# Kernel optimization log

Measured on AMD Instinct MI355X. Metric: run time of the kernel, lower is better.

Reference implementation:

```python
import jax, jax.numpy as jnp
import numpy as np

NB, NLOC, NALL, NNEI, A_SEL = 1, 512, 640, 96, 20
N_DIM, E_DIM, A_DIM, AXIS = 128, 64, 64, 4
EDGE_INFO = 2 * N_DIM + E_DIM          # 320
SYM = AXIS * (E_DIM + N_DIM)           # 768, cal_1_dim
ANGLE = A_DIM + N_DIM + 2 * E_DIM      # 320, angle_dim


def setup_inputs() -> dict:
    key = jax.random.key(0)
    ks = jax.random.split(key, 16)
    nrm = lambda k, sh, s=1.0: jax.random.normal(k, sh, dtype=jnp.float32) * s

    def lin(k, din, dout, s=0.05):
        k1, k2 = jax.random.split(k)
        return nrm(k1, (din, dout), s), nrm(k2, (dout,), s)

    inp = {}
    inp["g1_ext"] = nrm(ks[0], (NB, NALL, N_DIM))
    inp["g2"] = nrm(ks[1], (NB, NLOC, NNEI, E_DIM))
    inp["h2"] = nrm(ks[2], (NB, NLOC, NNEI, 3))
    inp["angle_embed"] = nrm(ks[3], (NB, NLOC, A_SEL, A_SEL, A_DIM))
    inp["sw"] = jax.random.uniform(ks[4], (NB, NLOC, NNEI), dtype=jnp.float32)
    inp["a_sw"] = jax.random.uniform(ks[5], (NB, NLOC, A_SEL), dtype=jnp.float32)
    inp["w_self"], inp["b_self"] = lin(ks[6], N_DIM, N_DIM)
    inp["w_proj"] = nrm(ks[7], (E_DIM, N_DIM), 0.05)  # proj_g1g2, bias=False
    inp["w_lin1"], inp["b_lin1"] = lin(ks[8], SYM, N_DIM)
    inp["w_edge1"], inp["b_edge1"] = lin(ks[9], EDGE_INFO, N_DIM)
    inp["w_lin2"], inp["b_lin2"] = lin(ks[10], EDGE_INFO, E_DIM)
    inp["w_ang"], inp["b_ang"] = lin(ks[11], ANGLE, A_DIM)
    inp["w_ga1"], inp["b_ga1"] = lin(ks[12], ANGLE, E_DIM)
    inp["w_ga2"], inp["b_ga2"] = lin(ks[13], E_DIM, E_DIM)
    inp["nlist"] = jax.random.randint(ks[14], (NB, NLOC, NNEI), 0, NALL)
    inp["nlist_mask"] = jnp.ones((NB, NLOC, NNEI), dtype=bool)
    inp["a_nlist_mask"] = jnp.ones((NB, NLOC, A_SEL), dtype=bool)
    return inp


def _sym_op(g, h2, mask, sw, axis):
    # symmetrization_op: _cal_hg (smooth, use_sqrt_nnei) followed by _cal_grrg
    # g: nb x nloc x nnei x d, h2: nb x nloc x nnei x 3
    g = jnp.where(mask[..., None], g, 0.0) * sw[..., None]
    inv = np.float32(1.0 / np.sqrt(g.shape[2]))
    hg = jnp.einsum('blnt,blnd->bltd', h2, g) * inv
    grrg = jnp.einsum('bltd,blta->blda', hg, hg[..., :axis])  # nb x nloc x d x axis
    return grrg.reshape(grrg.shape[0], grrg.shape[1], -1)


def reference(g1_ext, g2, h2, angle_embed, sw, a_sw,
              w_self, b_self, w_proj, w_lin1, b_lin1, w_edge1, b_edge1,
              w_lin2, b_lin2, w_ang, b_ang, w_ga1, b_ga1, w_ga2, b_ga2,
              nlist, nlist_mask, a_nlist_mask):
    act = jax.nn.silu
    nb, nloc, nnei, e_dim = g2.shape
    n_dim = g1_ext.shape[-1]
    a_sel = angle_embed.shape[2]
    g1 = g1_ext[:, :nloc]
    # _make_nei_g1: gather neighbor node features, nb x nloc x nnei x n_dim
    gg1 = jnp.take_along_axis(
        g1_ext, nlist.reshape(nb, nloc * nnei, 1), axis=1
    ).reshape(nb, nloc, nnei, n_dim)
    maskf = nlist_mask[..., None]
    swf = sw[..., None]

    g1_update = [g1]
    # node self mlp
    g1_update.append(act(g1 @ w_self + b_self))
    # conv update: masked+switched gg1 times projected g2, mean over nnei
    gg1_ms = jnp.where(maskf, gg1, 0.0) * swf
    g1_update.append(jnp.sum((g2 @ w_proj) * gg1_ms, axis=2) / np.float32(nnei))
    # symmetrized axis-neuron update
    sym = jnp.concatenate(
        [_sym_op(g2, h2, nlist_mask, sw, AXIS),
         _sym_op(gg1, h2, nlist_mask, sw, AXIS)], axis=-1)
    g1_update.append(act(sym @ w_lin1 + b_lin1))
    # edge info: [tiled g1, gg1, g2] -> 2*n_dim + e_dim
    edge_info = jnp.concatenate(
        [jnp.broadcast_to(g1[:, :, None, :], (nb, nloc, nnei, n_dim)), gg1, g2],
        axis=-1)
    g1_edge = act(edge_info @ w_edge1 + b_edge1) * swf
    g1_update.append(jnp.sum(g1_edge, axis=2) / np.float32(nnei))
    # res_avg
    g1_new = sum(g1_update) / np.float32(np.sqrt(len(g1_update)))

    g2_update = [g2, act(edge_info @ w_lin2 + b_lin2)]

    # angle branch: angle_dim = a_dim + n_dim + 2*e_dim
    g2a = jnp.where(a_nlist_mask[..., None], g2[:, :, :a_sel, :], 0.0)
    ang = jnp.concatenate([
        angle_embed,
        jnp.broadcast_to(g1[:, :, None, None, :], (nb, nloc, a_sel, a_sel, n_dim)),
        jnp.broadcast_to(g2a[:, :, :, None, :], (nb, nloc, a_sel, a_sel, e_dim)),
        jnp.broadcast_to(g2a[:, :, None, :, :], (nb, nloc, a_sel, a_sel, e_dim)),
    ], axis=-1)
    a_new = (angle_embed + act(ang @ w_ang + b_ang)) / np.float32(np.sqrt(2.0))

    # angle -> edge message, switch-weighted on both angle axes, mean over one axis
    ang_w = ang * a_sw[:, :, :, None, None] * a_sw[:, :, None, :, None]
    g2_ang = jnp.sum(act(ang_w @ w_ga1 + b_ga1), axis=3) / np.float32(a_sel)
    g2_ang_full = jnp.concatenate(
        [g2_ang, jnp.zeros((nb, nloc, nnei - a_sel, e_dim), g2.dtype)], axis=2)
    g2_update.append(act(g2_ang_full @ w_ga2 + b_ga2))
    g2_new = sum(g2_update) / np.float32(np.sqrt(len(g2_update)))

    return g1_new, g2_new, h2, a_new
```

## Files before the change

kernel.cpp:

```cpp
#include <hip/hip_runtime.h>
#include <hip/hip_bf16.h>

#define NLOC 512
#define NALL 640
#define NNEI 96
#define ASEL 20
#define NDIM 128
#define EDIM 64
#define ADIM 64

typedef short bf16x8 __attribute__((ext_vector_type(8)));
typedef float f32x4 __attribute__((ext_vector_type(4)));
typedef unsigned short ushort8 __attribute__((ext_vector_type(8)));
typedef unsigned short ushort4_t __attribute__((ext_vector_type(4)));

__device__ __forceinline__ unsigned short f2bf(float f) {
    unsigned int u = __float_as_uint(f);
    unsigned int r = (u + 0x7FFFu + ((u >> 16) & 1u)) >> 16;
    return (unsigned short)r;
}
__device__ __forceinline__ float bf2f(unsigned short u) {
    return __uint_as_float(((unsigned int)u) << 16);
}
__device__ __forceinline__ float silu(float x) { return x / (1.0f + __expf(-x)); }

__device__ __forceinline__ void cvt8_store(unsigned short* dst, const float* src) {
    float4 f0 = *(const float4*)src;
    float4 f1 = *(const float4*)(src + 4);
    ushort8 v;
    v[0] = f2bf(f0.x); v[1] = f2bf(f0.y); v[2] = f2bf(f0.z); v[3] = f2bf(f0.w);
    v[4] = f2bf(f1.x); v[5] = f2bf(f1.y); v[6] = f2bf(f1.z); v[7] = f2bf(f1.w);
    *(ushort8*)dst = v;
}

__global__ void prep_bt2(const float* __restrict__ w_ang, const float* __restrict__ w_ga1,
                         const float* __restrict__ w_edge1, const float* __restrict__ w_lin2,
                         const float* __restrict__ w_proj, const float* __restrict__ w_self,
                         unsigned short* __restrict__ bt_ae, unsigned short* __restrict__ bt_g2e,
                         unsigned short* __restrict__ bt_sm, unsigned short* __restrict__ bt_pij) {
    int idx = blockIdx.x * 256 + threadIdx.x;
    if (idx < 8192) {
        int k = idx & 63, n = idx >> 6;
        bt_ae[idx] = f2bf((n < 64) ? w_ang[k * 64 + n] : w_ga1[k * 64 + (n - 64)]);
    } else if (idx < 32768) {
        int id2 = idx - 8192;
        int k = id2 & 63, n = id2 >> 6;
        float v;
        if (n < 128)      v = w_edge1[(256 + k) * 128 + n];
        else if (n < 192) v = w_lin2[(256 + k) * 64 + (n - 128)];
        else if (n < 256) v = 0.0f;
        else              v = w_proj[k * 128 + (n - 256)];
        bt_g2e[id2] = f2bf(v);
    } else if (idx < 114688) {
        int id3 = idx - 32768;
        int k = id3 & 127, n = id3 >> 7;
        float v;
        if (n < 128)      v = w_edge1[k * 128 + n];
        else if (n < 192) v = w_lin2[k * 64 + (n - 128)];
        else if (n < 320) v = w_edge1[(128 + k) * 128 + (n - 192)];
        else if (n < 384) v = w_lin2[(128 + k) * 64 + (n - 320)];
        else if (n < 512) { int c = n - 384;
            v = (c < 64) ? w_ang[(64 + k) * 64 + c] : w_ga1[(64 + k) * 64 + (c - 64)]; }
        else              v = w_self[k * 128 + (n - 512)];
        bt_sm[id3] = f2bf(v);
    } else {
        int id4 = idx - 114688;
        int k = id4 & 63, n = id4 >> 6;
        float v;
        if (n < 128) v = (n < 64) ? w_ang[(192 + k) * 64 + n] : w_ga1[(192 + k) * 64 + (n - 64)];
        else { int c = n - 128;
            v = (c < 64) ? w_ang[(256 + k) * 64 + c] : w_ga1[(256 + k) * 64 + (c - 64)]; }
        bt_pij[id4] = f2bf(v);
    }
}

__global__ __launch_bounds__(256) void gemm_small(
    const float* __restrict__ g1_ext, const unsigned short* __restrict__ bt_sm,
    const float* __restrict__ b_self, float* __restrict__ P1a, float* __restrict__ g1self,
    float* __restrict__ E1, float* __restrict__ E2) {
    const int m0 = blockIdx.x * 128;
    const int ntile = blockIdx.y;
    __shared__ __align__(16) unsigned short Asl[128 * 136];
    __shared__ __align__(16) unsigned short Bsl[128 * 136];
    const int tid = threadIdx.x;
#pragma unroll
    for (int u = 0; u < 8; u++) {
        int g = tid + u * 256;
        int row = g >> 4, seg = g & 15;
        cvt8_store(&Asl[row * 136 + seg * 8], g1_ext + (m0 + row) * 128 + seg * 8);
        *(ushort8*)&Bsl[row * 136 + seg * 8] =
            *(const ushort8*)&bt_sm[(ntile * 128 + row) * 128 + seg * 8];
    }
    __syncthreads();
    const int lane = tid & 63, wid = tid >> 6;
    const int wr = wid >> 1, wc = wid & 1;
    const int r15 = lane & 15, kg = lane >> 4;
    f32x4 acc[4][4] = {};
#pragma unroll
    for (int h = 0; h < 4; h++) {
        bf16x8 afr[4], bfr[4];
#pragma unroll
        for (int mi = 0; mi < 4; mi++)
            afr[mi] = *(const bf16x8*)&Asl[(wr * 64 + mi * 16 + r15) * 136 + h * 32 + kg * 8];
#pragma unroll
        for (int ni = 0; ni < 4; ni++)
            bfr[ni] = *(const bf16x8*)&Bsl[(wc * 64 + ni * 16 + r15) * 136 + h * 32 + kg * 8];
#pragma unroll
        for (int mi = 0; mi < 4; mi++)
#pragma unroll
            for (int ni = 0; ni < 4; ni++)
                acc[mi][ni] = __builtin_amdgcn_mfma_f32_16x16x32_bf16(afr[mi], bfr[ni], acc[mi][ni], 0, 0, 0);
    }
#pragma unroll
    for (int mi = 0; mi < 4; mi++) {
        int rbase = m0 + wr * 64 + mi * 16 + kg * 4;
#pragma unroll
        for (int ni = 0; ni < 4; ni++) {
            int gc = ntile * 128 + wc * 64 + ni * 16 + r15;
#pragma unroll
            for (int t2 = 0; t2 < 4; t2++) {
                int a = rbase + t2;
                float z = acc[mi][ni][t2];
                if (gc < 192) { if (a < 512) E1[a * 192 + gc] = z; }
                else if (gc < 384) E2[a * 192 + (gc - 192)] = z;
                else if (gc < 512) { if (a < 512) P1a[a * 128 + (gc - 384)] = z; }
                else { if (a < 512) g1self[a * 128 + (gc - 512)] = silu(z + b_self[gc - 512]); }
            }
        }
    }
}

__global__ __launch_bounds__(256) void gemm_pij(
    const float* __restrict__ g2, const unsigned short* __restrict__ bt_pij,
    unsigned short* __restrict__ P_i, unsigned short* __restrict__ P_j,
    unsigned short* __restrict__ P_jT) {
    const int m0 = blockIdx.x * 128;
    const int ntile = blockIdx.y;
    __shared__ __align__(16) unsigned short Asl[128 * 72];
    const int tid = threadIdx.x;
#pragma unroll
    for (int u = 0; u < 4; u++) {
        int g = tid + u * 256;
        int row = g >> 3, seg = g & 7;
        int li = m0 + row, l = li / 20, i = li - l * 20;
        cvt8_store(&Asl[row * 72 + seg * 8], g2 + (l * 96 + i) * 64 + seg * 8);
    }
    __syncthreads();
    const int lane = tid & 63, wid = tid >> 6;
    const int wr = wid >> 1, wc = wid & 1;
    const int r15 = lane & 15, kg = lane >> 4;
    f32x4 acc[4][4] = {};
#pragma unroll
    for (int h = 0; h < 2; h++) {
        bf16x8 afr[4], bfr[4];
#pragma unroll
        for (int mi = 0; mi < 4; mi++)
            afr[mi] = *(const bf16x8*)&Asl[(wr * 64 + mi * 16 + r15) * 72 + h * 32 + kg * 8];
#pragma unroll
        for (int ni = 0; ni < 4; ni++)
            bfr[ni] = *(const bf16x8*)&bt_pij[(ntile * 128 + wc * 64 + ni * 16 + r15) * 64 + h * 32 + kg * 8];
#pragma unroll
        for (int mi = 0; mi < 4; mi++)
#pragma unroll
            for (int ni = 0; ni < 4; ni++)
                acc[mi][ni] = __builtin_amdgcn_mfma_f32_16x16x32_bf16(afr[mi], bfr[ni], acc[mi][ni], 0, 0, 0);
    }
    unsigned short* Pout = (ntile == 0) ? P_i : P_j;
#pragma unroll
    for (int mi = 0; mi < 4; mi++) {
        int rbase = m0 + wr * 64 + mi * 16 + kg * 4;
#pragma unroll
        for (int ni = 0; ni < 4; ni++) {
            int c = wc * 64 + ni * 16 + r15;
#pragma unroll
            for (int t2 = 0; t2 < 4; t2++) {
                unsigned short v = f2bf(acc[mi][ni][t2]);
                int li = rbase + t2;
                Pout[li * 128 + c] = v;
                if (ntile == 1) {
                    int l = li / 20, j = li - l * 20;
                    P_jT[(l * 128 + c) * 20 + j] = v;
                }
            }
        }
    }
}

__global__ void k_sym(const float* __restrict__ g1_ext, const float* __restrict__ g2,
                      const float* __restrict__ h2, const float* __restrict__ sw,
                      const int* __restrict__ nlist, const float* __restrict__ w_lin1,
                      const float* __restrict__ b_lin1, float* __restrict__ term4) {
    int l = blockIdx.x, t = threadIdx.x;
    __shared__ float h2s[96 * 3];
    __shared__ float sws[96];
    __shared__ int nls[96];
    __shared__ float hg[3 * 192];
    __shared__ float symv[768];
    __shared__ float red[128];
    if (t < 96) { sws[t] = sw[l * 96 + t]; nls[t] = nlist[l * 96 + t]; }
    for (int p = t; p < 288; p += 256) h2s[p] = h2[l * 288 + p];
    __syncthreads();
    const float inv = 0.1020620726f;
    for (int p = t; p < 576; p += 256) {
        float acc = 0.0f;
        if (p < 192) {
            int tt = p >> 6, d = p & 63;
            for (int n = 0; n < 96; n++)
                acc += h2s[n * 3 + tt] * g2[(l * 96 + n) * 64 + d] * sws[n];
            hg[tt * 192 + d] = acc * inv;
        } else {
            int q = p - 192;
            int tt = q >> 7, d = q & 127;
            for (int n = 0; n < 96; n++)
                acc += h2s[n * 3 + tt] * g1_ext[nls[n] * 128 + d] * sws[n];
            hg[tt * 192 + 64 + d] = acc * inv;
        }
    }
    __syncthreads();
    for (int p = t; p < 768; p += 256) {
        float acc = 0.0f;
        if (p < 256) {
            int d = p >> 2, a = p & 3;
            for (int tt = 0; tt < 3; tt++) acc += hg[tt * 192 + d] * hg[tt * 192 + a];
        } else {
            int q = p - 256;
            int d = q >> 2, a = q & 3;
            for (int tt = 0; tt < 3; tt++) acc += hg[tt * 192 + 64 + d] * hg[tt * 192 + 64 + a];
        }
        symv[p] = acc;
    }
    __syncthreads();
    {
        int col = t & 127, half = t >> 7;
        float acc = 0.0f;
        int k0 = half * 384;
#pragma unroll 8
        for (int k = k0; k < k0 + 384; k++) acc += symv[k] * w_lin1[k * 128 + col];
        if (half) red[col] = acc;
        __syncthreads();
        if (!half) term4[l * 128 + col] = silu(acc + red[col] + b_lin1[col]);
    }
}

__global__ __launch_bounds__(256) void angle_main(
    const float* __restrict__ ae, const unsigned short* __restrict__ bt_ae,
    const float* __restrict__ P1a, const unsigned short* __restrict__ P_i,
    const unsigned short* __restrict__ P_j, const unsigned short* __restrict__ P_jT,
    const float* __restrict__ a_sw,
    const float* __restrict__ b_ang, const float* __restrict__ b_ga1,
    float* __restrict__ g2acc, float* __restrict__ a_new_out) {
    const int m0 = blockIdx.x * 128;
    __shared__ __align__(16) unsigned short Asl[128 * 72];
    const int tid = threadIdx.x;
#pragma unroll
    for (int u = 0; u < 4; u++) {
        int g = tid + u * 256;
        int row = g >> 3, seg = g & 7;
        cvt8_store(&Asl[row * 72 + seg * 8], ae + (m0 + row) * 64 + seg * 8);
    }
    __syncthreads();
    const int lane = tid & 63, wid = tid >> 6;
    const int r15 = lane & 15, kg = lane >> 4;
    f32x4 accA[2][4] = {};
    f32x4 accB[2][4] = {};
#pragma unroll
    for (int h = 0; h < 2; h++) {
        bf16x8 afr[2], bfrA[4], bfrB[4];
#pragma unroll
        for (int mi = 0; mi < 2; mi++)
            afr[mi] = *(const bf16x8*)&Asl[(wid * 32 + mi * 16 + r15) * 72 + h * 32 + kg * 8];
#pragma unroll
        for (int ni = 0; ni < 4; ni++) {
            bfrA[ni] = *(const bf16x8*)&bt_ae[(ni * 16 + r15) * 64 + h * 32 + kg * 8];
            bfrB[ni] = *(const bf16x8*)&bt_ae[(64 + ni * 16 + r15) * 64 + h * 32 + kg * 8];
        }
#pragma unroll
        for (int mi = 0; mi < 2; mi++)
#pragma unroll
            for (int ni = 0; ni < 4; ni++) {
                accA[mi][ni] = __builtin_amdgcn_mfma_f32_16x16x32_bf16(bfrA[ni], afr[mi], accA[mi][ni], 0, 0, 0);
                accB[mi][ni] = __builtin_amdgcn_mfma_f32_16x16x32_bf16(afr[mi], bfrB[ni], accB[mi][ni], 0, 0, 0);
            }
    }
#pragma unroll
    for (int mi = 0; mi < 2; mi++) {
        int r = m0 + wid * 32 + mi * 16 + r15;
        int l = r / 400;
        int rem = r - l * 400;
        int i = rem / 20;
        int j = rem - i * 20;
        const float* p1b = P1a + l * 128;
        const unsigned short* pib = P_i + (l * 20 + i) * 128;
        const unsigned short* pjb = P_j + (l * 20 + j) * 128;
        int lr = r - m0;
#pragma unroll
        for (int ni = 0; ni < 4; ni++) {
            int n0 = ni * 16 + kg * 4;
            f32x4 p1v = *(const f32x4*)&p1b[n0];
            ushort4_t piv = *(const ushort4_t*)&pib[n0];
            ushort4_t pjv = *(const ushort4_t*)&pjb[n0];
            ushort4_t aev = *(const ushort4_t*)&Asl[lr * 72 + n0];
            f32x4 bbv = *(const f32x4*)&b_ang[n0];
            f32x4 outv;
#pragma unroll
            for (int t2 = 0; t2 < 4; t2++) {
                float z = accA[mi][ni][t2] + p1v[t2] + bf2f(piv[t2]) + bf2f(pjv[t2]);
                outv[t2] = (bf2f(aev[t2]) + silu(z + bbv[t2])) * 0.70710678f;
            }
            *(f32x4*)&a_new_out[r * 64 + n0] = outv;
        }
    }
#pragma unroll
    for (int mi = 0; mi < 2; mi++) {
        int rbase = m0 + wid * 32 + mi * 16 + kg * 4;
        int l = rbase / 400;
        int rem = rbase - l * 400;
        int i = rem / 20;
        int j0 = rem - i * 20;
        const float* p1b = P1a + l * 128;
        const unsigned short* pib = P_i + (l * 20 + i) * 128;
        float swi = a_sw[l * 20 + i];
        f32x4 swjv = *(const f32x4*)&a_sw[l * 20 + j0];
#pragma unroll
        for (int ni = 0; ni < 4; ni++) {
            int c = 64 + ni * 16 + r15;
            int cc = c - 64;
            float base = p1b[c] + bf2f(pib[c]);
            float bb = b_ga1[cc];
            ushort4_t pjtv = *(const ushort4_t*)&P_jT[(l * 128 + c) * 20 + j0];
            float part = 0.0f;
#pragma unroll
            for (int t2 = 0; t2 < 4; t2++) {
                float z = accB[mi][ni][t2] + base + bf2f(pjtv[t2]);
                part += silu(swi * swjv[t2] * z + bb);
            }
            atomicAdd(&g2acc[(l * 20 + i) * 64 + cc], part);
        }
    }
}

__global__ void k_f2(const float* __restrict__ g2ang_acc, const float* __restrict__ w_ga2,
                     const float* __restrict__ b_ga2, float* __restrict__ yga2) {
    int l = blockIdx.x, t = threadIdx.x;
    __shared__ float gs[20 * 64];
    for (int p = t; p < 1280; p += 256) gs[p] = g2ang_acc[l * 1280 + p] * 0.05f;
    __syncthreads();
    for (int p = t; p < 1280; p += 256) {
        int i = p >> 6, c = p & 63;
        float acc = b_ga2[c];
#pragma unroll 8
        for (int k = 0; k < 64; k++) acc += gs[i * 64 + k] * w_ga2[k * 64 + c];
        yga2[l * 1280 + p] = silu(acc);
    }
}

__global__ __launch_bounds__(256) void edge_main(
    const float* __restrict__ g1_ext, const float* __restrict__ g2, const float* __restrict__ sw,
    const int* __restrict__ nlist, const unsigned short* __restrict__ bt_g2e,
    const float* __restrict__ E1, const float* __restrict__ E2,
    const float* __restrict__ b_edge1, const float* __restrict__ b_lin2,
    const float* __restrict__ b_ga2, const float* __restrict__ yga2,
    float* __restrict__ g1_acc3, float* __restrict__ g1_acc5, float* __restrict__ g2_new_out) {
    const int m0 = blockIdx.x * 128;
    const int ntile = blockIdx.y;
    __shared__ __align__(16) unsigned short Asl[128 * 72];
    const int tid = threadIdx.x;
#pragma unroll
    for (int u = 0; u < 4; u++) {
        int g = tid + u * 256;
        int row = g >> 3, seg = g & 7;
        cvt8_store(&Asl[row * 72 + seg * 8], g2 + (m0 + row) * 64 + seg * 8);
    }
    __syncthreads();
    const int lane = tid & 63, wid = tid >> 6;
    const int r15 = lane & 15, kg = lane >> 4;
    if (ntile == 1) {
        f32x4 acc[2][4] = {};
#pragma unroll
        for (int h = 0; h < 2; h++) {
            bf16x8 afr[2], bfr[4];
#pragma unroll
            for (int mi = 0; mi < 2; mi++)
                afr[mi] = *(const bf16x8*)&Asl[(wid * 32 + mi * 16 + r15) * 72 + h * 32 + kg * 8];
#pragma unroll
            for (int ni = 0; ni < 4; ni++)
                bfr[ni] = *(const bf16x8*)&bt_g2e[(128 + ni * 16 + r15) * 64 + h * 32 + kg * 8];
#pragma unroll
            for (int mi = 0; mi < 2; mi++)
#pragma unroll
                for (int ni = 0; ni < 4; ni++)
                    acc[mi][ni] = __builtin_amdgcn_mfma_f32_16x16x32_bf16(bfr[ni], afr[mi], acc[mi][ni], 0, 0, 0);
        }
#pragma unroll
        for (int mi = 0; mi < 2; mi++) {
            int r = m0 + wid * 32 + mi * 16 + r15;
            int l = r / 96;
            int nn = r - l * 96;
            const float* e1 = E1 + l * 192 + 128;
            const float* e2 = E2 + nlist[r] * 192 + 128;
            bool hasyg = (nn < ASEL);
            const float* yg = yga2 + (l * 20 + nn) * 64;
            int lr = r - m0;
#pragma unroll
            for (int ni = 0; ni < 4; ni++) {
                int n0 = ni * 16 + kg * 4;
                f32x4 e1v = *(const f32x4*)&e1[n0];
                f32x4 e2v = *(const f32x4*)&e2[n0];
                f32x4 bbv = *(const f32x4*)&b_lin2[n0];
                f32x4 bg2 = *(const f32x4*)&b_ga2[n0];
                ushort4_t g2v = *(const ushort4_t*)&Asl[lr * 72 + n0];
                f32x4 outv;
#pragma unroll
                for (int t2 = 0; t2 < 4; t2++) {
                    float z = acc[mi][ni][t2] + e1v[t2] + e2v[t2];
                    float y = silu(z + bbv[t2]);
                    float ygv = hasyg ? yg[n0 + t2] : silu(bg2[t2]);
                    outv[t2] = (bf2f(g2v[t2]) + y + ygv) * 0.57735027f;
                }
                *(f32x4*)&g2_new_out[r * 64 + n0] = outv;
            }
        }
    } else {
        const int wr = wid >> 1, wc = wid & 1;
        f32x4 acc[4][4] = {};
#pragma unroll
        for (int h = 0; h < 2; h++) {
            bf16x8 afr[4], bfr[4];
#pragma unroll
            for (int mi = 0; mi < 4; mi++)
                afr[mi] = *(const bf16x8*)&Asl[(wr * 64 + mi * 16 + r15) * 72 + h * 32 + kg * 8];
#pragma unroll
            for (int ni = 0; ni < 4; ni++)
                bfr[ni] = *(const bf16x8*)&bt_g2e[(ntile * 128 + wc * 64 + ni * 16 + r15) * 64 + h * 32 + kg * 8];
#pragma unroll
            for (int mi = 0; mi < 4; mi++)
#pragma unroll
                for (int ni = 0; ni < 4; ni++)
                    acc[mi][ni] = __builtin_amdgcn_mfma_f32_16x16x32_bf16(afr[mi], bfr[ni], acc[mi][ni], 0, 0, 0);
        }
#pragma unroll
        for (int mi = 0; mi < 4; mi++) {
            int rbase = m0 + wr * 64 + mi * 16 + kg * 4;
            int l = rbase / 96;
#pragma unroll
            for (int ni = 0; ni < 4; ni++) {
                int c = wc * 64 + ni * 16 + r15;
                if (ntile == 0) {
                    float e1 = E1[l * 192 + c];
                    float bb = b_edge1[c];
                    float part = 0.0f;
#pragma unroll
                    for (int t2 = 0; t2 < 4; t2++) {
                        int r = rbase + t2;
                        float z = acc[mi][ni][t2] + e1 + E2[nlist[r] * 192 + c];
                        part += silu(z + bb) * sw[r];
                    }
                    atomicAdd(&g1_acc5[l * 128 + c], part);
                } else {
                    float part = 0.0f;
#pragma unroll
                    for (int t2 = 0; t2 < 4; t2++) {
                        int r = rbase + t2;
                        part += acc[mi][ni][t2] * g1_ext[nlist[r] * 128 + c] * sw[r];
                    }
                    atomicAdd(&g1_acc3[l * 128 + c], part);
                }
            }
        }
    }
}

__global__ void k_f1(const float* __restrict__ g1_ext, const float* __restrict__ g1self,
                     const float* __restrict__ acc3, const float* __restrict__ term4,
                     const float* __restrict__ acc5, float* __restrict__ out_g1) {
    int idx = blockIdx.x * 256 + threadIdx.x;
    float v = g1_ext[idx] + g1self[idx] + acc3[idx] * (1.0f / 96.0f) + term4[idx] +
              acc5[idx] * (1.0f / 96.0f);
    out_g1[idx] = v * 0.4472135955f;
}

extern "C" void kernel_launch(void* const* d_in, const int* in_sizes, int n_in,
                              void* d_out, int out_size, void* d_ws, size_t ws_size,
                              hipStream_t stream) {
    if (n_in < 22 || in_sizes[0] != 81920 || in_sizes[3] != 13107200) return;
    const float* g1_ext = (const float*)d_in[0];
    const float* g2     = (const float*)d_in[1];
    const float* h2     = (const float*)d_in[2];
    const float* ae     = (const float*)d_in[3];
    const float* sw     = (const float*)d_in[4];
    const float* a_sw   = (const float*)d_in[5];
    const float* w_self = (const float*)d_in[6];
    const float* b_self = (const float*)d_in[7];
    const float* w_proj = (const float*)d_in[8];
    const float* w_lin1 = (const float*)d_in[9];
    const float* b_lin1 = (const float*)d_in[10];
    const float* w_edge1= (const float*)d_in[11];
    const float* b_edge1= (const float*)d_in[12];
    const float* w_lin2 = (const float*)d_in[13];
    const float* b_lin2 = (const float*)d_in[14];
    const float* w_ang  = (const float*)d_in[15];
    const float* b_ang  = (const float*)d_in[16];
    const float* w_ga1  = (const float*)d_in[17];
    const float* b_ga1  = (const float*)d_in[18];
    const float* w_ga2  = (const float*)d_in[19];
    const float* b_ga2  = (const float*)d_in[20];
    const int*   nlist  = (const int*)d_in[21];

    float* ws = (float*)d_ws;
    unsigned short* bt_ae  = (unsigned short*)(ws);
    unsigned short* bt_g2e = (unsigned short*)(ws + 4096);
    unsigned short* bt_sm  = (unsigned short*)(ws + 16384);
    unsigned short* bt_pij = (unsigned short*)(ws + 57344);
    float* P1a    = ws + 65536;
    float* E1     = ws + 131072;
    float* E2     = ws + 229376;
    unsigned short* P_i = (unsigned short*)(ws + 352256);
    unsigned short* P_j = (unsigned short*)(ws + 1007616);
    float* g1self = ws + 1662976;
    float* term4  = ws + 1728512;
    float* yga2   = ws + 1794048;
    float* acc3   = ws + 2449408;
    float* acc5   = ws + 2514944;
    float* g2acc  = ws + 2580480;
    unsigned short* P_jT = (unsigned short*)(ws + 3235840);
    if (ws_size < (size_t)3563520 * sizeof(float)) return;

    float* out = (float*)d_out;
    float* out_g1 = out;
    float* out_g2 = out + 65536;
    float* out_h2 = out + 3211264;
    float* out_an = out + 3358720;

    hipMemsetAsync(acc3, 0, (65536 + 65536 + 655360) * sizeof(float), stream);

    prep_bt2<<<512, 256, 0, stream>>>(w_ang, w_ga1, w_edge1, w_lin2, w_proj, w_self,
                                      bt_ae, bt_g2e, bt_sm, bt_pij);
    gemm_small<<<dim3(5, 5), 256, 0, stream>>>(g1_ext, bt_sm, b_self, P1a, g1self, E1, E2);
    gemm_pij<<<dim3(80, 2), 256, 0, stream>>>(g2, bt_pij, P_i, P_j, P_jT);
    k_sym<<<512, 256, 0, stream>>>(g1_ext, g2, h2, sw, nlist, w_lin1, b_lin1, term4);
    angle_main<<<1600, 256, 0, stream>>>(ae, bt_ae, P1a, P_i, P_j, P_jT, a_sw, b_ang, b_ga1,
                                         g2acc, out_an);
    k_f2<<<512, 256, 0, stream>>>(g2acc, w_ga2, b_ga2, yga2);
    edge_main<<<dim3(384, 3), 256, 0, stream>>>(g1_ext, g2, sw, nlist, bt_g2e, E1, E2,
                                                b_edge1, b_lin2, b_ga2, yga2,
                                                acc3, acc5, out_g2);
    k_f1<<<256, 256, 0, stream>>>(g1_ext, g1self, acc3, term4, acc5, out_g1);
    hipMemcpyAsync(out_h2, h2, 147456 * sizeof(float), hipMemcpyDeviceToDevice, stream);
}
```

Baseline: 178.4 us.

## Split angle kernel into ga1 and a_new passes, fold h2 copy into k_f1

The fused angle kernel becomes two kernels. One computes the g2-angle message with atomics, and the other computes a_new later in the stream, so k_f2 and edge_main's dependency resolves earlier. The h2 passthrough copy moves into k_f1 in place of a separate memcpy. In exchange, the large angle_embed input is read and converted twice and there is one more launch.

```diff
diff --git a/kernel.cpp b/kernel.cpp
--- a/kernel.cpp
+++ b/kernel.cpp
@@ -242,13 +242,11 @@
     }
 }
 
-__global__ __launch_bounds__(256) void angle_main(
+__global__ __launch_bounds__(256) void k_ga1(
     const float* __restrict__ ae, const unsigned short* __restrict__ bt_ae,
     const float* __restrict__ P1a, const unsigned short* __restrict__ P_i,
-    const unsigned short* __restrict__ P_j, const unsigned short* __restrict__ P_jT,
-    const float* __restrict__ a_sw,
-    const float* __restrict__ b_ang, const float* __restrict__ b_ga1,
-    float* __restrict__ g2acc, float* __restrict__ a_new_out) {
+    const unsigned short* __restrict__ P_jT, const float* __restrict__ a_sw,
+    const float* __restrict__ b_ga1, float* __restrict__ g2acc) {
     const int m0 = blockIdx.x * 128;
     __shared__ __align__(16) unsigned short Asl[128 * 72];
     const int tid = threadIdx.x;
@@ -261,26 +259,83 @@
     __syncthreads();
     const int lane = tid & 63, wid = tid >> 6;
     const int r15 = lane & 15, kg = lane >> 4;
-    f32x4 accA[2][4] = {};
     f32x4 accB[2][4] = {};
 #pragma unroll
     for (int h = 0; h < 2; h++) {
-        bf16x8 afr[2], bfrA[4], bfrB[4];
+        bf16x8 afr[2], bfrB[4];
 #pragma unroll
         for (int mi = 0; mi < 2; mi++)
             afr[mi] = *(const bf16x8*)&Asl[(wid * 32 + mi * 16 + r15) * 72 + h * 32 + kg * 8];
 #pragma unroll
+        for (int ni = 0; ni < 4; ni++)
+            bfrB[ni] = *(const bf16x8*)&bt_ae[(64 + ni * 16 + r15) * 64 + h * 32 + kg * 8];
+#pragma unroll
+        for (int mi = 0; mi < 2; mi++)
+#pragma unroll
+            for (int ni = 0; ni < 4; ni++)
+                accB[mi][ni] = __builtin_amdgcn_mfma_f32_16x16x32_bf16(afr[mi], bfrB[ni], accB[mi][ni], 0, 0, 0);
+    }
+#pragma unroll
+    for (int mi = 0; mi < 2; mi++) {
+        int rbase = m0 + wid * 32 + mi * 16 + kg * 4;
+        int l = rbase / 400;
+        int rem = rbase - l * 400;
+        int i = rem / 20;
+        int j0 = rem - i * 20;
+        const float* p1b = P1a + l * 128;
+        const unsigned short* pib = P_i + (l * 20 + i) * 128;
+        float swi = a_sw[l * 20 + i];
+        f32x4 swjv = *(const f32x4*)&a_sw[l * 20 + j0];
+#pragma unroll
         for (int ni = 0; ni < 4; ni++) {
+            int c = 64 + ni * 16 + r15;
+            int cc = c - 64;
+            float base = p1b[c] + bf2f(pib[c]);
+            float bb = b_ga1[cc];
+            ushort4_t pjtv = *(const ushort4_t*)&P_jT[(l * 128 + c) * 20 + j0];
+            float part = 0.0f;
+#pragma unroll
+            for (int t2 = 0; t2 < 4; t2++) {
+                float z = accB[mi][ni][t2] + base + bf2f(pjtv[t2]);
+                part += silu(swi * swjv[t2] * z + bb);
+            }
+            atomicAdd(&g2acc[(l * 20 + i) * 64 + cc], part);
+        }
+    }
+}
+
+__global__ __launch_bounds__(256) void k_anew(
+    const float* __restrict__ ae, const unsigned short* __restrict__ bt_ae,
+    const float* __restrict__ P1a, const unsigned short* __restrict__ P_i,
+    const unsigned short* __restrict__ P_j, const float* __restrict__ b_ang,
+    float* __restrict__ a_new_out) {
+    const int m0 = blockIdx.x * 128;
+    __shared__ __align__(16) unsigned short Asl[128 * 72];
+    const int tid = threadIdx.x;
+#pragma unroll
+    for (int u = 0; u < 4; u++) {
+        int g = tid + u * 256;
+        int row = g >> 3, seg = g & 7;
+        cvt8_store(&Asl[row * 72 + seg * 8], ae + (m0 + row) * 64 + seg * 8);
+    }
+    __syncthreads();
+    const int lane = tid & 63, wid = tid >> 6;
+    const int r15 = lane & 15, kg = lane >> 4;
+    f32x4 accA[2][4] = {};
+#pragma unroll
+    for (int h = 0; h < 2; h++) {
+        bf16x8 afr[2], bfrA[4];
+#pragma unroll
+        for (int mi = 0; mi < 2; mi++)
+            afr[mi] = *(const bf16x8*)&Asl[(wid * 32 + mi * 16 + r15) * 72 + h * 32 + kg * 8];
+#pragma unroll
+        for (int ni = 0; ni < 4; ni++)
             bfrA[ni] = *(const bf16x8*)&bt_ae[(ni * 16 + r15) * 64 + h * 32 + kg * 8];
-            bfrB[ni] = *(const bf16x8*)&bt_ae[(64 + ni * 16 + r15) * 64 + h * 32 + kg * 8];
-        }
 #pragma unroll
         for (int mi = 0; mi < 2; mi++)
 #pragma unroll
-            for (int ni = 0; ni < 4; ni++) {
+            for (int ni = 0; ni < 4; ni++)
                 accA[mi][ni] = __builtin_amdgcn_mfma_f32_16x16x32_bf16(bfrA[ni], afr[mi], accA[mi][ni], 0, 0, 0);
-                accB[mi][ni] = __builtin_amdgcn_mfma_f32_16x16x32_bf16(afr[mi], bfrB[ni], accB[mi][ni], 0, 0, 0);
-            }
     }
 #pragma unroll
     for (int mi = 0; mi < 2; mi++) {
@@ -308,33 +363,6 @@
                 outv[t2] = (bf2f(aev[t2]) + silu(z + bbv[t2])) * 0.70710678f;
             }
             *(f32x4*)&a_new_out[r * 64 + n0] = outv;
-        }
-    }
-#pragma unroll
-    for (int mi = 0; mi < 2; mi++) {
-        int rbase = m0 + wid * 32 + mi * 16 + kg * 4;
-        int l = rbase / 400;
-        int rem = rbase - l * 400;
-        int i = rem / 20;
-        int j0 = rem - i * 20;
-        const float* p1b = P1a + l * 128;
-        const unsigned short* pib = P_i + (l * 20 + i) * 128;
-        float swi = a_sw[l * 20 + i];
-        f32x4 swjv = *(const f32x4*)&a_sw[l * 20 + j0];
-#pragma unroll
-        for (int ni = 0; ni < 4; ni++) {
-            int c = 64 + ni * 16 + r15;
-            int cc = c - 64;
-            float base = p1b[c] + bf2f(pib[c]);
-            float bb = b_ga1[cc];
-            ushort4_t pjtv = *(const ushort4_t*)&P_jT[(l * 128 + c) * 20 + j0];
-            float part = 0.0f;
-#pragma unroll
-            for (int t2 = 0; t2 < 4; t2++) {
-                float z = accB[mi][ni][t2] + base + bf2f(pjtv[t2]);
-                part += silu(swi * swjv[t2] * z + bb);
-            }
-            atomicAdd(&g2acc[(l * 20 + i) * 64 + cc], part);
         }
     }
 }
@@ -472,11 +500,14 @@
 
 __global__ void k_f1(const float* __restrict__ g1_ext, const float* __restrict__ g1self,
                      const float* __restrict__ acc3, const float* __restrict__ term4,
-                     const float* __restrict__ acc5, float* __restrict__ out_g1) {
+                     const float* __restrict__ acc5, const float* __restrict__ h2,
+                     float* __restrict__ out_g1, float* __restrict__ out_h2) {
     int idx = blockIdx.x * 256 + threadIdx.x;
     float v = g1_ext[idx] + g1self[idx] + acc3[idx] * (1.0f / 96.0f) + term4[idx] +
               acc5[idx] * (1.0f / 96.0f);
     out_g1[idx] = v * 0.4472135955f;
+    if (idx < 36864)
+        *(float4*)&out_h2[idx * 4] = *(const float4*)&h2[idx * 4];
 }
 
 extern "C" void kernel_launch(void* const* d_in, const int* in_sizes, int n_in,
@@ -537,13 +568,12 @@
                                       bt_ae, bt_g2e, bt_sm, bt_pij);
     gemm_small<<<dim3(5, 5), 256, 0, stream>>>(g1_ext, bt_sm, b_self, P1a, g1self, E1, E2);
     gemm_pij<<<dim3(80, 2), 256, 0, stream>>>(g2, bt_pij, P_i, P_j, P_jT);
+    k_ga1<<<1600, 256, 0, stream>>>(ae, bt_ae, P1a, P_i, P_jT, a_sw, b_ga1, g2acc);
+    k_f2<<<512, 256, 0, stream>>>(g2acc, w_ga2, b_ga2, yga2);
     k_sym<<<512, 256, 0, stream>>>(g1_ext, g2, h2, sw, nlist, w_lin1, b_lin1, term4);
-    angle_main<<<1600, 256, 0, stream>>>(ae, bt_ae, P1a, P_i, P_j, P_jT, a_sw, b_ang, b_ga1,
-                                         g2acc, out_an);
-    k_f2<<<512, 256, 0, stream>>>(g2acc, w_ga2, b_ga2, yga2);
     edge_main<<<dim3(384, 3), 256, 0, stream>>>(g1_ext, g2, sw, nlist, bt_g2e, E1, E2,
                                                 b_edge1, b_lin2, b_ga2, yga2,
                                                 acc3, acc5, out_g2);
-    k_f1<<<256, 256, 0, stream>>>(g1_ext, g1self, acc3, term4, acc5, out_g1);
-    hipMemcpyAsync(out_h2, h2, 147456 * sizeof(float), hipMemcpyDeviceToDevice, stream);
-}
+    k_anew<<<1600, 256, 0, stream>>>(ae, bt_ae, P1a, P_i, P_j, b_ang, out_an);
+    k_f1<<<256, 256, 0, stream>>>(g1_ext, g1self, acc3, term4, acc5, h2, out_g1, out_h2);
+}
```

After: 190.1 us. 6.5% more time.

## Transpose edge MFMA tiles, reduce rows by shuffle, fuse h2 copy into k_f1

Applied to the files above, without the earlier changes.

The edge_main g1-reduction path swaps the MFMA operand order so each lane owns one row and four contiguous columns. This allows vectorised E1/E2/g1_ext loads, a 16-lane shuffle reduction over rows sharing an atom, and far fewer global atomics. The h2 passthrough copy moves from a separate hipMemcpyAsync into the final k_f1 kernel, which removes one stream operation. The code assumes 16 consecutive rows share the same atom index l, which holds because 96 is a multiple of 16. It adds shuffle work in exchange.

```diff
diff --git a/kernel.cpp b/kernel.cpp
--- a/kernel.cpp
+++ b/kernel.cpp
@@ -31,6 +31,17 @@
     v[0] = f2bf(f0.x); v[1] = f2bf(f0.y); v[2] = f2bf(f0.z); v[3] = f2bf(f0.w);
     v[4] = f2bf(f1.x); v[5] = f2bf(f1.y); v[6] = f2bf(f1.z); v[7] = f2bf(f1.w);
     *(ushort8*)dst = v;
+}
+
+__device__ __forceinline__ f32x4 red16(f32x4 v) {
+#pragma unroll
+    for (int m = 1; m < 16; m <<= 1) {
+        v[0] += __shfl_xor(v[0], m);
+        v[1] += __shfl_xor(v[1], m);
+        v[2] += __shfl_xor(v[2], m);
+        v[3] += __shfl_xor(v[3], m);
+    }
+    return v;
 }
 
 __global__ void prep_bt2(const float* __restrict__ w_ang, const float* __restrict__ w_ga1,
@@ -421,49 +432,65 @@
             }
         }
     } else {
-        const int wr = wid >> 1, wc = wid & 1;
-        f32x4 acc[4][4] = {};
+        const int bn = (ntile == 0) ? 0 : 256;
+        f32x4 acc[2][8] = {};
 #pragma unroll
         for (int h = 0; h < 2; h++) {
-            bf16x8 afr[4], bfr[4];
-#pragma unroll
-            for (int mi = 0; mi < 4; mi++)
-                afr[mi] = *(const bf16x8*)&Asl[(wr * 64 + mi * 16 + r15) * 72 + h * 32 + kg * 8];
-#pragma unroll
-            for (int ni = 0; ni < 4; ni++)
-                bfr[ni] = *(const bf16x8*)&bt_g2e[(ntile * 128 + wc * 64 + ni * 16 + r15) * 64 + h * 32 + kg * 8];
-#pragma unroll
-            for (int mi = 0; mi < 4; mi++)
-#pragma unroll
-                for (int ni = 0; ni < 4; ni++)
-                    acc[mi][ni] = __builtin_amdgcn_mfma_f32_16x16x32_bf16(afr[mi], bfr[ni], acc[mi][ni], 0, 0, 0);
-        }
-#pragma unroll
-        for (int mi = 0; mi < 4; mi++) {
-            int rbase = m0 + wr * 64 + mi * 16 + kg * 4;
-            int l = rbase / 96;
-#pragma unroll
-            for (int ni = 0; ni < 4; ni++) {
-                int c = wc * 64 + ni * 16 + r15;
-                if (ntile == 0) {
-                    float e1 = E1[l * 192 + c];
-                    float bb = b_edge1[c];
-                    float part = 0.0f;
-#pragma unroll
-                    for (int t2 = 0; t2 < 4; t2++) {
-                        int r = rbase + t2;
-                        float z = acc[mi][ni][t2] + e1 + E2[nlist[r] * 192 + c];
-                        part += silu(z + bb) * sw[r];
+            bf16x8 afr[2], bfr[8];
+#pragma unroll
+            for (int mi = 0; mi < 2; mi++)
+                afr[mi] = *(const bf16x8*)&Asl[(wid * 32 + mi * 16 + r15) * 72 + h * 32 + kg * 8];
+#pragma unroll
+            for (int ni = 0; ni < 8; ni++)
+                bfr[ni] = *(const bf16x8*)&bt_g2e[(bn + ni * 16 + r15) * 64 + h * 32 + kg * 8];
+#pragma unroll
+            for (int mi = 0; mi < 2; mi++)
+#pragma unroll
+                for (int ni = 0; ni < 8; ni++)
+                    acc[mi][ni] = __builtin_amdgcn_mfma_f32_16x16x32_bf16(bfr[ni], afr[mi], acc[mi][ni], 0, 0, 0);
+        }
+#pragma unroll
+        for (int mi = 0; mi < 2; mi++) {
+            int r = m0 + wid * 32 + mi * 16 + r15;
+            int l = r / 96;
+            float swr = sw[r];
+            int nr = nlist[r];
+            if (ntile == 0) {
+                const float* e1 = E1 + l * 192;
+                const float* e2 = E2 + nr * 192;
+#pragma unroll
+                for (int ni = 0; ni < 8; ni++) {
+                    int n0 = ni * 16 + kg * 4;
+                    f32x4 e1v = *(const f32x4*)&e1[n0];
+                    f32x4 e2v = *(const f32x4*)&e2[n0];
+                    f32x4 bbv = *(const f32x4*)&b_edge1[n0];
+                    f32x4 p;
+#pragma unroll
+                    for (int t2 = 0; t2 < 4; t2++)
+                        p[t2] = silu(acc[mi][ni][t2] + e1v[t2] + e2v[t2] + bbv[t2]) * swr;
+                    p = red16(p);
+                    if (r15 == 0) {
+#pragma unroll
+                        for (int t2 = 0; t2 < 4; t2++)
+                            atomicAdd(&g1_acc5[l * 128 + n0 + t2], p[t2]);
                     }
-                    atomicAdd(&g1_acc5[l * 128 + c], part);
-                } else {
-                    float part = 0.0f;
-#pragma unroll
-                    for (int t2 = 0; t2 < 4; t2++) {
-                        int r = rbase + t2;
-                        part += acc[mi][ni][t2] * g1_ext[nlist[r] * 128 + c] * sw[r];
+                }
+            } else {
+                const float* gv = g1_ext + nr * 128;
+#pragma unroll
+                for (int ni = 0; ni < 8; ni++) {
+                    int n0 = ni * 16 + kg * 4;
+                    f32x4 g4 = *(const f32x4*)&gv[n0];
+                    f32x4 p;
+#pragma unroll
+                    for (int t2 = 0; t2 < 4; t2++)
+                        p[t2] = acc[mi][ni][t2] * g4[t2] * swr;
+                    p = red16(p);
+                    if (r15 == 0) {
+#pragma unroll
+                        for (int t2 = 0; t2 < 4; t2++)
+                            atomicAdd(&g1_acc3[l * 128 + n0 + t2], p[t2]);
                     }
-                    atomicAdd(&g1_acc3[l * 128 + c], part);
                 }
             }
         }
@@ -472,11 +499,14 @@
 
 __global__ void k_f1(const float* __restrict__ g1_ext, const float* __restrict__ g1self,
                      const float* __restrict__ acc3, const float* __restrict__ term4,
-                     const float* __restrict__ acc5, float* __restrict__ out_g1) {
+                     const float* __restrict__ acc5, const float* __restrict__ h2,
+                     float* __restrict__ out_g1, float* __restrict__ out_h2) {
     int idx = blockIdx.x * 256 + threadIdx.x;
     float v = g1_ext[idx] + g1self[idx] + acc3[idx] * (1.0f / 96.0f) + term4[idx] +
               acc5[idx] * (1.0f / 96.0f);
     out_g1[idx] = v * 0.4472135955f;
+    if (idx < 36864)
+        *(float4*)&out_h2[idx * 4] = *(const float4*)&h2[idx * 4];
 }
 
 extern "C" void kernel_launch(void* const* d_in, const int* in_sizes, int n_in,
@@ -544,6 +574,5 @@
     edge_main<<<dim3(384, 3), 256, 0, stream>>>(g1_ext, g2, sw, nlist, bt_g2e, E1, E2,
                                                 b_edge1, b_lin2, b_ga2, yga2,
                                                 acc3, acc5, out_g2);
-    k_f1<<<256, 256, 0, stream>>>(g1_ext, g1self, acc3, term4, acc5, out_g1);
-    hipMemcpyAsync(out_h2, h2, 147456 * sizeof(float), hipMemcpyDeviceToDevice, stream);
-}
+    k_f1<<<256, 256, 0, stream>>>(g1_ext, g1self, acc3, term4, acc5, h2, out_g1, out_h2);
+}
```

New measurement: 166.0 us, median of 2. -6.9%, faster.
